# Kernel tuning notes

Hardware: AMD Instinct MI355X
Metric: run time of the kernel (lower is better)

The kernel has to match this reference:

```python
import jax, jax.numpy as jnp
import numpy as np

GAMMA, ALPHA = 2.0, 0.25
MATCH_THR, BKG_THR = 0.5, 0.4  # fastai match_anchors defaults
SCALE = jnp.array([0.1, 0.1, 0.2, 0.2], dtype=jnp.float32)


def cthw2tlbr(b):
    c, s = b[..., :2], b[..., 2:]
    return jnp.concatenate([c - s / 2, c + s / 2], -1)


def tlbr2cthw(b):
    tl, br = b[..., :2], b[..., 2:]
    return jnp.concatenate([(tl + br) / 2, br - tl], -1)


def iou_cthw(anc, tgt):
    # anc [A,4], tgt [T,4], cthw -> [A,T]
    a, t = cthw2tlbr(anc), cthw2tlbr(tgt)
    tl = jnp.maximum(a[:, None, :2], t[None, :, :2])
    br = jnp.minimum(a[:, None, 2:], t[None, :, 2:])
    sz = jnp.clip(br - tl, 0.0)
    inter = sz[..., 0] * sz[..., 1]
    union = (anc[:, 2] * anc[:, 3])[:, None] + (tgt[:, 2] * tgt[:, 3])[None, :] - inter
    return inter / (union + 1e-8)


def one_image(cp, bp, ct, bt, anchors):
    # cp [A,C], bp [A,4], ct [T] int (0 = pad/background id), bt [T,4] tlbr
    n_classes = cp.shape[1]
    bt_cthw = tlbr2cthw(bt)
    ious = iou_cthw(anchors, bt_cthw)                       # [A,T]
    vals, idxs = jnp.max(ious, 1), jnp.argmax(ious, 1)
    matches = jnp.where(vals > MATCH_THR, idxs,
                        jnp.where(vals < BKG_THR, -1, -2))  # -2 = ignore
    bbox_mask = matches >= 0
    m = jnp.sum(bbox_mask)
    mf = m.astype(cp.dtype)
    g = bt_cthw[jnp.clip(matches, 0)]                       # [A,4] gathered tgt cthw
    t_ctr = (g[:, :2] - anchors[:, :2]) / anchors[:, 2:]
    t_sz = jnp.log(g[:, 2:] / anchors[:, 2:] + 1e-8)
    activ = jnp.concatenate([t_ctr, t_sz], -1) / SCALE
    d = bp - activ
    huber = jnp.where(jnp.abs(d) < 1.0, 0.5 * d * d, jnp.abs(d) - 0.5)
    bb_loss = jnp.sum(huber * bbox_mask[:, None]) / jnp.maximum(mf * 4.0, 1.0)
    # classification: background (0) for matches==-1, gathered class for matches>=0
    cls = jnp.where(bbox_mask, ct[jnp.clip(matches, 0)], 0)  # [A]
    clas_mask = (matches >= -1).astype(cp.dtype)             # drop ignored anchors
    tgt = jax.nn.one_hot(cls - 1, n_classes, dtype=cp.dtype) # cls==0 -> all-zero row
    ps = jax.nn.sigmoid(cp)
    w = (tgt * (1 - ps) + (1 - tgt) * ps) ** GAMMA * ((1 - tgt) * ALPHA + tgt * (1 - ALPHA))
    bce = tgt * jax.nn.softplus(-cp) + (1 - tgt) * jax.nn.softplus(cp)
    focal = jnp.sum(w * bce * clas_mask[:, None]) / jnp.maximum(mf, 1.0)
    return bb_loss, focal


def setup_inputs() -> dict:
    key = jax.random.key(0)
    B, A, C, T = 16, 49152, 80, 64
    k1, k2, k3, k4, k5, k6, k7 = jax.random.split(key, 7)
    clas_preds = jax.random.normal(k1, (B, A, C), jnp.float32)
    bbox_preds = jax.random.normal(k2, (B, A, 4), jnp.float32)
    xy1 = jax.random.uniform(k3, (B, T, 2)) * 0.7
    wh = jax.random.uniform(k4, (B, T, 2)) * 0.25 + 0.02
    bbox_tgts = jnp.concatenate([xy1, xy1 + wh], -1)        # tlbr, all valid
    clas_tgts = jax.random.randint(k5, (B, T), 1, C + 1)    # no padding (>=1)
    ctr = jax.random.uniform(k6, (A, 2))
    sz = jax.random.uniform(k7, (A, 2)) * 0.25 + 0.02
    anchors = jnp.concatenate([ctr, sz], -1)                # cthw
    return dict(clas_preds=clas_preds, bbox_preds=bbox_preds,
                bbox_tgts=bbox_tgts, clas_tgts=clas_tgts, anchors=anchors)


def reference(clas_preds, bbox_preds, bbox_tgts, clas_tgts, anchors):
    bb, fl = jax.vmap(lambda cp, bp, ct, bt: one_image(cp, bp, ct, bt, anchors))(
        clas_preds, bbox_preds, clas_tgts, bbox_tgts)
    return (jnp.sum(bb) + jnp.sum(fl)) / clas_preds.shape[0]
```

## Files before the change

### kernel.cpp

```cpp
#include <hip/hip_runtime.h>


#define A_CNT 49152
#define T_CNT 64
#define C_CNT 80
#define ABLK  256
#define NBLK  (A_CNT / ABLK)
#define B_CNT 16
#define NSLOT (B_CNT * NBLK)

#define LN2   0.6931471806f
#define RLN2  1.44269504f

typedef float f32x4 __attribute__((ext_vector_type(4)));

__device__ __forceinline__ float focal4q(f32x4 v) {
    float e0 = __builtin_amdgcn_exp2f(v.x * RLN2);
    float e1 = __builtin_amdgcn_exp2f(v.y * RLN2);
    float e2 = __builtin_amdgcn_exp2f(v.z * RLN2);
    float e3 = __builtin_amdgcn_exp2f(v.w * RLN2);
    float t0 = 1.0f + e0, t1 = 1.0f + e1, t2 = 1.0f + e2, t3 = 1.0f + e3;
    float t01 = t0 * t1, t23 = t2 * t3;
    float r   = __builtin_amdgcn_rcpf(t01 * t23);
    float r01 = r * t23, r23 = r * t01;
    float s0 = e0 * (r01 * t1);
    float s1 = e1 * (r01 * t0);
    float s2 = e2 * (r23 * t3);
    float s3 = e3 * (r23 * t2);
    float L0 = __builtin_amdgcn_logf(t0);
    float L1 = __builtin_amdgcn_logf(t1);
    float L2 = __builtin_amdgcn_logf(t2);
    float L3 = __builtin_amdgcn_logf(t3);
    return ((s0 * s0) * L0 + (s1 * s1) * L1)
         + ((s2 * s2) * L2 + (s3 * s3) * L3);
}

__global__ __launch_bounds__(ABLK) void rnfl_main(
    const float* __restrict__ clas_preds,
    const float* __restrict__ bbox_preds,
    const float* __restrict__ bbox_tgts,
    const int*   __restrict__ clas_tgts,
    const float* __restrict__ anchors,
    float* __restrict__ bb_part,
    float* __restrict__ fl_part,
    float* __restrict__ m_part)
{
    const int tid  = threadIdx.x;
    const int g    = blockIdx.x;
    const int lane = tid & 63, wave = tid >> 6;
    const int b    = g / NBLK;
    const int bx   = g - b * NBLK;
    const int a0   = bx * ABLK;

    __shared__ float4 tbox[T_CNT];
    __shared__ float  taT[T_CNT];
    __shared__ int    tcl[T_CNT];
    __shared__ int    codes[ABLK];
    __shared__ float  rv[4][4];

    const f32x4* cp4 = reinterpret_cast<const f32x4*>(clas_preds)
                     + ((size_t)b * A_CNT + a0) * (C_CNT / 4);

    f32x4 buf[8];
#pragma unroll
    for (int i = 0; i < 8; ++i)
        buf[i] = cp4[i * ABLK + tid];

    if (tid < T_CNT) {
        float4 bt = reinterpret_cast<const float4*>(bbox_tgts)[b * T_CNT + tid];
        float cx = (bt.x + bt.z) * 0.5f;
        float cy = (bt.y + bt.w) * 0.5f;
        float sx = bt.z - bt.x;
        float sy = bt.w - bt.y;
        float4 tb;
        tb.x = cx - sx * 0.5f;
        tb.y = cy - sy * 0.5f;
        tb.z = cx + sx * 0.5f;
        tb.w = cy + sy * 0.5f;
        tbox[tid] = tb;
        taT[tid]  = sx * sy + 1e-8f;
        tcl[tid]  = clas_tgts[b * T_CNT + tid];
    }
    __syncthreads();

    const int a = a0 + tid;
    float4 anc = reinterpret_cast<const float4*>(anchors)[a];
    const float ax1 = anc.x - anc.z * 0.5f;
    const float ay1 = anc.y - anc.w * 0.5f;
    const float ax2 = anc.x + anc.z * 0.5f;
    const float ay2 = anc.y + anc.w * 0.5f;
    const float areaA = anc.z * anc.w;

    float bn = -1.0f, bd = 1.0f;
    int   bj = 0;
#pragma unroll 8
    for (int j = 0; j < T_CNT; ++j) {
        float4 tb = tbox[j];
        float ix1 = fmaxf(ax1, tb.x);
        float iy1 = fmaxf(ay1, tb.y);
        float ix2 = fminf(ax2, tb.z);
        float iy2 = fminf(ay2, tb.w);
        float w = fmaxf(ix2 - ix1, 0.0f);
        float h = fmaxf(iy2 - iy1, 0.0f);
        float inter = w * h;
        float den = (areaA + taT[j]) - inter;
        if (inter * bd > bn * den) { bn = inter; bd = den; bj = j; }
    }

    int   code;
    float bb   = 0.0f;
    float flc  = 0.0f;
    float mloc = 0.0f;

    if (bn > 0.5f * bd) {
        mloc = 1.0f;
        code = tcl[bj] - 1;
        float4 tb = tbox[bj];
        float gx = (tb.x + tb.z) * 0.5f;
        float gy = (tb.y + tb.w) * 0.5f;
        float gw = tb.z - tb.x;
        float gh = tb.w - tb.y;
        float4 bp = reinterpret_cast<const float4*>(bbox_preds)[(size_t)b * A_CNT + a];
        float t0 = ((gx - anc.x) / anc.z) * 10.0f;
        float t1 = ((gy - anc.y) / anc.w) * 10.0f;
        float t2 = __logf(gw / anc.z + 1e-8f) * 5.0f;
        float t3 = __logf(gh / anc.w + 1e-8f) * 5.0f;
        float d, ad;
        d = bp.x - t0; ad = fabsf(d); bb += (ad < 1.0f) ? 0.5f * d * d : ad - 0.5f;
        d = bp.y - t1; ad = fabsf(d); bb += (ad < 1.0f) ? 0.5f * d * d : ad - 0.5f;
        d = bp.z - t2; ad = fabsf(d); bb += (ad < 1.0f) ? 0.5f * d * d : ad - 0.5f;
        d = bp.w - t3; ad = fabsf(d); bb += (ad < 1.0f) ? 0.5f * d * d : ad - 0.5f;

        float x  = clas_preds[((size_t)b * A_CNT + a) * C_CNT + code];
        float e  = __builtin_amdgcn_exp2f(x * RLN2);
        float t  = 1.0f + e;
        float inv = __builtin_amdgcn_rcpf(t);
        float ps = e * inv;
        float q  = 1.0f - ps;
        float L  = __builtin_amdgcn_logf(t);
        float sp = LN2 * L;
        flc = 0.75f * q * q * (sp - x) - 0.25f * ps * ps * sp;
    } else {
        code = (bn >= 0.4f * bd) ? -2 : -1;
    }
    codes[tid] = code;
    __syncthreads();

    unsigned mbits = 0;
#pragma unroll
    for (int k = 0; k < 20; ++k) {
        int al = (unsigned)(k * ABLK + tid) / 20u;
        mbits |= (codes[al] >= -1 ? 1u : 0u) << k;
    }

    float acc = 0.0f;
#pragma unroll
    for (int k = 0; k < 12; ++k) {
        f32x4 cur = buf[k & 7];
        buf[k & 7] = cp4[(k + 8) * ABLK + tid];
        float m = (float)((mbits >> k) & 1u);
        acc = fmaf(m, focal4q(cur), acc);
    }
#pragma unroll
    for (int k = 12; k < 20; ++k) {
        float m = (float)((mbits >> k) & 1u);
        acc = fmaf(m, focal4q(buf[k & 7]), acc);
    }
    float fl = fmaf(acc, 0.25f * LN2, flc);

#pragma unroll
    for (int off = 32; off > 0; off >>= 1) {
        bb   += __shfl_down(bb, off);
        fl   += __shfl_down(fl, off);
        mloc += __shfl_down(mloc, off);
    }
    if (lane == 0) { rv[wave][0] = bb; rv[wave][1] = fl; rv[wave][2] = mloc; }
    __syncthreads();
    if (tid == 0) {
        int slot = b * NBLK + bx;
        bb_part[slot] = rv[0][0] + rv[1][0] + rv[2][0] + rv[3][0];
        fl_part[slot] = rv[0][1] + rv[1][1] + rv[2][1] + rv[3][1];
        m_part[slot]  = rv[0][2] + rv[1][2] + rv[2][2] + rv[3][2];
    }
}

__global__ __launch_bounds__(256) void rnfl_final(
    const float* __restrict__ bb_part,
    const float* __restrict__ fl_part,
    const float* __restrict__ m_part,
    float* __restrict__ out)
{
    __shared__ float bbL[NSLOT], flL[NSLOT], mL[NSLOT];
    __shared__ float wacc[4];
    const int tid = threadIdx.x, lane = tid & 63, wave = tid >> 6;

#pragma unroll
    for (int k = 0; k < NSLOT / 256; ++k) {
        int s = k * 256 + tid;
        bbL[s] = bb_part[s];
        flL[s] = fl_part[s];
        mL[s]  = m_part[s];
    }
    __syncthreads();

    float lacc = 0.0f;
    for (int img = wave; img < B_CNT; img += 4) {
        float bb = 0.0f, fl = 0.0f, m = 0.0f;
#pragma unroll
        for (int s = 0; s < 3; ++s) {
            int i = img * NBLK + s * 64 + lane;
            bb += bbL[i];
            fl += flL[i];
            m  += mL[i];
        }
#pragma unroll
        for (int off = 32; off > 0; off >>= 1) {
            bb += __shfl_down(bb, off);
            fl += __shfl_down(fl, off);
            m  += __shfl_down(m, off);
        }
        if (lane == 0)
            lacc += bb / fmaxf(m * 4.0f, 1.0f) + fl / fmaxf(m, 1.0f);
    }
    if (lane == 0) wacc[wave] = lacc;
    __syncthreads();
    if (tid == 0)
        out[0] = (wacc[0] + wacc[1] + wacc[2] + wacc[3]) / (float)B_CNT;
}

extern "C" void kernel_launch(void* const* d_in, const int* in_sizes, int n_in,
                              void* d_out, int out_size, void* d_ws, size_t ws_size,
                              hipStream_t stream)
{
    const float* clas_preds = (const float*)d_in[0];
    const float* bbox_preds = (const float*)d_in[1];
    const float* bbox_tgts  = (const float*)d_in[2];
    const int*   clas_tgts  = (const int*)d_in[3];
    const float* anchors    = (const float*)d_in[4];
    float* out = (float*)d_out;

    float* bb_part = (float*)d_ws;
    float* fl_part = bb_part + NSLOT;
    float* m_part  = fl_part + NSLOT;

    rnfl_main<<<NSLOT, ABLK, 0, stream>>>(clas_preds, bbox_preds, bbox_tgts,
                                          clas_tgts, anchors,
                                          bb_part, fl_part, m_part);
    rnfl_final<<<1, 256, 0, stream>>>(bb_part, fl_part, m_part, out);
}
```

Baseline: 56.94 us.

## Pack IoU and focal math into float2 ops and fold hot-class fix into stream

Splits the target boxes into struct-of-arrays float2 shared arrays so the IoU argmax loop processes two targets per iteration with packed float2 min/max/mul ops. It keeps two running best matches and merges them with a tie-break that preserves the lowest index. The scattered per-anchor reload of the matched class logit is removed; the positive-class correction is now computed from the already-loaded vector when a thread's chunk contains the matched class. The focal inner math is also expressed in float2 to encourage packed FP32 instructions. The cost is extra shared reads of codes and a divergent branch inside the streaming loop.

```diff
diff --git a/kernel.cpp b/kernel.cpp
--- a/kernel.cpp
+++ b/kernel.cpp
@@ -13,26 +13,35 @@
 #define RLN2  1.44269504f
 
 typedef float f32x4 __attribute__((ext_vector_type(4)));
+typedef float f32x2 __attribute__((ext_vector_type(2)));
 
 __device__ __forceinline__ float focal4q(f32x4 v) {
     float e0 = __builtin_amdgcn_exp2f(v.x * RLN2);
     float e1 = __builtin_amdgcn_exp2f(v.y * RLN2);
     float e2 = __builtin_amdgcn_exp2f(v.z * RLN2);
     float e3 = __builtin_amdgcn_exp2f(v.w * RLN2);
-    float t0 = 1.0f + e0, t1 = 1.0f + e1, t2 = 1.0f + e2, t3 = 1.0f + e3;
-    float t01 = t0 * t1, t23 = t2 * t3;
+    f32x2 eA = {e0, e1}, eB = {e2, e3};
+    f32x2 tA = eA + 1.0f, tB = eB + 1.0f;
+    float t01 = tA.x * tA.y, t23 = tB.x * tB.y;
     float r   = __builtin_amdgcn_rcpf(t01 * t23);
-    float r01 = r * t23, r23 = r * t01;
-    float s0 = e0 * (r01 * t1);
-    float s1 = e1 * (r01 * t0);
-    float s2 = e2 * (r23 * t3);
-    float s3 = e3 * (r23 * t2);
-    float L0 = __builtin_amdgcn_logf(t0);
-    float L1 = __builtin_amdgcn_logf(t1);
-    float L2 = __builtin_amdgcn_logf(t2);
-    float L3 = __builtin_amdgcn_logf(t3);
-    return ((s0 * s0) * L0 + (s1 * s1) * L1)
-         + ((s2 * s2) * L2 + (s3 * s3) * L3);
+    float p   = r * t23, q = r * t01;
+    f32x2 invA = (f32x2){p, p} * (f32x2){tA.y, tA.x};
+    f32x2 invB = (f32x2){q, q} * (f32x2){tB.y, tB.x};
+    f32x2 sA = eA * invA, sB = eB * invB;
+    f32x2 LA = { __builtin_amdgcn_logf(tA.x), __builtin_amdgcn_logf(tA.y) };
+    f32x2 LB = { __builtin_amdgcn_logf(tB.x), __builtin_amdgcn_logf(tB.y) };
+    f32x2 a2 = (sA * sA) * LA + (sB * sB) * LB;
+    return a2.x + a2.y;
+}
+
+__device__ __forceinline__ float hotfix(f32x4 cur, unsigned d) {
+    float x = (d == 0) ? cur.x : (d == 1) ? cur.y : (d == 2) ? cur.z : cur.w;
+    float e  = __builtin_amdgcn_exp2f(x * RLN2);
+    float t  = 1.0f + e;
+    float inv = __builtin_amdgcn_rcpf(t);
+    float ps = e * inv, qq = 1.0f - ps;
+    float sp = LN2 * __builtin_amdgcn_logf(t);
+    return 0.75f * qq * qq * (sp - x) - 0.25f * ps * ps * sp;
 }
 
 __global__ __launch_bounds__(ABLK) void rnfl_main(
@@ -53,7 +62,9 @@
     const int a0   = bx * ABLK;
 
     __shared__ float4 tbox[T_CNT];
-    __shared__ float  taT[T_CNT];
+    __shared__ f32x2  tX1v[T_CNT / 2], tY1v[T_CNT / 2];
+    __shared__ f32x2  tX2v[T_CNT / 2], tY2v[T_CNT / 2];
+    __shared__ f32x2  tSv[T_CNT / 2];
     __shared__ int    tcl[T_CNT];
     __shared__ int    codes[ABLK];
     __shared__ float  rv[4][4];
@@ -78,8 +89,12 @@
         tb.z = cx + sx * 0.5f;
         tb.w = cy + sy * 0.5f;
         tbox[tid] = tb;
-        taT[tid]  = sx * sy + 1e-8f;
-        tcl[tid]  = clas_tgts[b * T_CNT + tid];
+        ((float*)tX1v)[tid] = tb.x;
+        ((float*)tY1v)[tid] = tb.y;
+        ((float*)tX2v)[tid] = tb.z;
+        ((float*)tY2v)[tid] = tb.w;
+        ((float*)tSv)[tid]  = sx * sy + 1e-8f;
+        tcl[tid] = clas_tgts[b * T_CNT + tid];
     }
     __syncthreads();
 
@@ -90,26 +105,34 @@
     const float ax2 = anc.x + anc.z * 0.5f;
     const float ay2 = anc.y + anc.w * 0.5f;
     const float areaA = anc.z * anc.w;
-
-    float bn = -1.0f, bd = 1.0f;
-    int   bj = 0;
-#pragma unroll 8
-    for (int j = 0; j < T_CNT; ++j) {
-        float4 tb = tbox[j];
-        float ix1 = fmaxf(ax1, tb.x);
-        float iy1 = fmaxf(ay1, tb.y);
-        float ix2 = fminf(ax2, tb.z);
-        float iy2 = fminf(ay2, tb.w);
-        float w = fmaxf(ix2 - ix1, 0.0f);
-        float h = fmaxf(iy2 - iy1, 0.0f);
-        float inter = w * h;
-        float den = (areaA + taT[j]) - inter;
-        if (inter * bd > bn * den) { bn = inter; bd = den; bj = j; }
-    }
+    const f32x2 A1 = {ax1, ax1}, B1 = {ay1, ay1};
+    const f32x2 A2 = {ax2, ax2}, B2 = {ay2, ay2};
+    const f32x2 SA = {areaA, areaA};
+    const f32x2 Z  = {0.0f, 0.0f};
+
+    float bnX = -1.0f, bdX = 1.0f;
+    float bnY = -1.0f, bdY = 1.0f;
+    int   bjx = 0, bjy = 1;
+#pragma unroll 4
+    for (int p = 0; p < T_CNT / 2; ++p) {
+        f32x2 ix1 = __builtin_elementwise_max(A1, tX1v[p]);
+        f32x2 iy1 = __builtin_elementwise_max(B1, tY1v[p]);
+        f32x2 ix2 = __builtin_elementwise_min(A2, tX2v[p]);
+        f32x2 iy2 = __builtin_elementwise_min(B2, tY2v[p]);
+        f32x2 w = __builtin_elementwise_max(ix2 - ix1, Z);
+        f32x2 h = __builtin_elementwise_max(iy2 - iy1, Z);
+        f32x2 interV = w * h;
+        f32x2 denV = (SA + tSv[p]) - interV;
+        if (interV.x * bdX > bnX * denV.x) { bnX = interV.x; bdX = denV.x; bjx = 2 * p; }
+        if (interV.y * bdY > bnY * denV.y) { bnY = interV.y; bdY = denV.y; bjy = 2 * p + 1; }
+    }
+    float vx = bnX * bdY, vy = bnY * bdX;
+    float bn, bd; int bj;
+    if (vx > vy || (vx == vy && bjx < bjy)) { bn = bnX; bd = bdX; bj = bjx; }
+    else                                    { bn = bnY; bd = bdY; bj = bjy; }
 
     int   code;
     float bb   = 0.0f;
-    float flc  = 0.0f;
     float mloc = 0.0f;
 
     if (bn > 0.5f * bd) {
@@ -130,43 +153,38 @@
         d = bp.y - t1; ad = fabsf(d); bb += (ad < 1.0f) ? 0.5f * d * d : ad - 0.5f;
         d = bp.z - t2; ad = fabsf(d); bb += (ad < 1.0f) ? 0.5f * d * d : ad - 0.5f;
         d = bp.w - t3; ad = fabsf(d); bb += (ad < 1.0f) ? 0.5f * d * d : ad - 0.5f;
-
-        float x  = clas_preds[((size_t)b * A_CNT + a) * C_CNT + code];
-        float e  = __builtin_amdgcn_exp2f(x * RLN2);
-        float t  = 1.0f + e;
-        float inv = __builtin_amdgcn_rcpf(t);
-        float ps = e * inv;
-        float q  = 1.0f - ps;
-        float L  = __builtin_amdgcn_logf(t);
-        float sp = LN2 * L;
-        flc = 0.75f * q * q * (sp - x) - 0.25f * ps * ps * sp;
     } else {
         code = (bn >= 0.4f * bd) ? -2 : -1;
     }
     codes[tid] = code;
     __syncthreads();
 
-    unsigned mbits = 0;
-#pragma unroll
-    for (int k = 0; k < 20; ++k) {
-        int al = (unsigned)(k * ABLK + tid) / 20u;
-        mbits |= (codes[al] >= -1 ? 1u : 0u) << k;
-    }
-
     float acc = 0.0f;
+    float hot = 0.0f;
 #pragma unroll
     for (int k = 0; k < 12; ++k) {
         f32x4 cur = buf[k & 7];
         buf[k & 7] = cp4[(k + 8) * ABLK + tid];
-        float m = (float)((mbits >> k) & 1u);
+        int f  = k * ABLK + tid;
+        int al = (unsigned)f / 20u;
+        int cc = codes[al];
+        float m = (cc >= -1) ? 1.0f : 0.0f;
         acc = fmaf(m, focal4q(cur), acc);
+        unsigned d = (unsigned)(cc - (f - al * 20) * 4);
+        if (d < 4u) hot += hotfix(cur, d);
     }
 #pragma unroll
     for (int k = 12; k < 20; ++k) {
-        float m = (float)((mbits >> k) & 1u);
-        acc = fmaf(m, focal4q(buf[k & 7]), acc);
-    }
-    float fl = fmaf(acc, 0.25f * LN2, flc);
+        f32x4 cur = buf[k & 7];
+        int f  = k * ABLK + tid;
+        int al = (unsigned)f / 20u;
+        int cc = codes[al];
+        float m = (cc >= -1) ? 1.0f : 0.0f;
+        acc = fmaf(m, focal4q(cur), acc);
+        unsigned d = (unsigned)(cc - (f - al * 20) * 4);
+        if (d < 4u) hot += hotfix(cur, d);
+    }
+    float fl = fmaf(acc, 0.25f * LN2, hot);
 
 #pragma unroll
     for (int off = 32; off > 0; off >>= 1) {
```

Measured after the change: 67.63 us. 18.8% more time.
